# Kernel tuning notes

Hardware: AMD Instinct MI355X
Metric: run time of the kernel (lower is better)

## Reference

```python
import jax, jax.numpy as jnp
import numpy as np

N, D, C, T = 8192, 64, 100, 30  # samples, embedding_dim, n_classes, n_transforms (initialize_radial_flow n_transforms=30)
LOG_EV_CLAMP = 10.0             # EvidenceScaler clamp on log evidence
EV_BUDGET = 0.5 * D * float(np.log(4.0 * np.pi))  # 'normal' evidence budget: 0.5*dim*log(4*pi)


def setup_inputs() -> dict:
    key = jax.random.key(0)
    ks = jax.random.split(key, 8)
    x = jax.random.normal(ks[0], (N, D), dtype=jnp.float32)          # embeddings (base = identity here)
    labels = jax.random.randint(ks[1], (N,), 0, C)                   # int class labels
    freq = jax.random.uniform(ks[2], (C,), dtype=jnp.float32) + 0.1
    freq = freq / freq.sum()                                         # labels_frequency (sums to 1)
    # per-class radial flow params: z0 [C,T,D], alpha' [C,T], beta' [C,T]
    z0 = jax.random.normal(ks[3], (C, T, D), dtype=jnp.float32) * 0.1
    alpha_prime = jax.random.normal(ks[4], (C, T), dtype=jnp.float32) * 0.1
    beta_prime = jax.random.normal(ks[5], (C, T), dtype=jnp.float32) * 0.1
    W = jax.random.normal(ks[6], (D, C), dtype=jnp.float32) / np.sqrt(D)  # CategoricalOutput linear
    b = jnp.zeros((C,), jnp.float32)
    return dict(x=x, labels=labels, labels_frequency=freq, z0=z0,
                alpha_prime=alpha_prime, beta_prime=beta_prime, W=W, b=b)


def _flow_log_prob(x, z0s, aps, bps):
    """Radial normalizing flow log-density (density direction): log N(f(x)) + log|det df/dx|.
    x: [N, D]; z0s: [T, D]; aps, bps: [T]."""
    def step(carry, params):
        z, ld = carry
        z0, ap, bp = params
        alpha = jax.nn.softplus(ap)
        beta = -alpha + jax.nn.softplus(bp)   # beta > -alpha ensures invertibility
        diff = z - z0                          # [N, D]
        r = jnp.linalg.norm(diff, axis=-1)     # [N]
        h = 1.0 / (alpha + r)
        bh = beta * h
        z_new = z + bh[:, None] * diff
        # log|det| = (D-1)*log(1+beta*h) + log(1 + beta*h + beta*h'*r), h' = -h^2
        ld_new = ld + (D - 1) * jnp.log1p(bh) + jnp.log1p(bh * (1.0 - h * r))
        return (z_new, ld_new), None

    init = (x, jnp.zeros(x.shape[0], x.dtype))
    (z, ld), _ = jax.lax.scan(step, init, (z0s, aps, bps))
    base = -0.5 * (D * jnp.log(2.0 * jnp.pi) + jnp.sum(z * z, axis=-1))  # standard normal base
    return base + ld


def reference(x, labels, labels_frequency, z0, alpha_prime, beta_prime, W, b):
    # per-class flow log-probs for ALL samples: [C, N] (dispatch-compute, vectorized over classes)
    lp = jax.vmap(_flow_log_prob, in_axes=(None, 0, 0, 0))(x, z0, alpha_prime, beta_prime)
    # class_specific_log_prob: gather each sample's own-class log-prob (the boolean-mask gather/scatter loop)
    class_lp = jnp.take_along_axis(lp, labels[None, :], axis=0)[0]            # [N]
    # marginalize_log_prob: logsumexp over classes with log class frequencies
    marg = jax.nn.logsumexp(lp + jnp.log(labels_frequency)[:, None], axis=0)  # [N]
    # EvidenceScaler('normal') + clamp, then NatPN Dirichlet posterior update
    log_ev = jnp.minimum(marg + EV_BUDGET, LOG_EV_CLAMP)                      # [N]
    probs = jax.nn.softmax(x @ W + b, axis=-1)                                # expected sufficient statistics
    alpha = 1.0 + jnp.exp(log_ev)[:, None] * probs                            # prior alpha=1 + evidence*stats
    # output: [N, C+1] = [log alpha | class-specific log-prob]
    return jnp.concatenate([jnp.log(alpha), class_lp[:, None]], axis=1)
```

## Files before the change

### kernel.cpp

```cpp
#include <hip/hip_runtime.h>
#include <math.h>

#define N 8192
#define D 64
#define C 100
#define T 30
#define GSTRIDE 32
#define ZROWS 32
#define CROWS 112
#define WSTRIDE 20
#define SB 16

static constexpr float D_LOG_2PI      = 117.62413225019811f;
static constexpr float EV_BUDGET_F    = 80.992775903017304f;
static constexpr float LOG_EV_CLAMP_F = 10.0f;

typedef __attribute__((ext_vector_type(8))) short short8x;
typedef __attribute__((ext_vector_type(4))) float floatx4;

static __device__ __forceinline__ unsigned short f2bf(float f) {
    __bf16 h = (__bf16)f;
    return __builtin_bit_cast(unsigned short, h);
}

__global__ __launch_bounds__(256) void megaprep_kernel(
        const float* __restrict__ x,
        const float* __restrict__ z0,
        const float* __restrict__ ap,
        const float* __restrict__ bp,
        const float* __restrict__ W,
        unsigned short* __restrict__ xbf,
        float* __restrict__ q0,
        float* __restrict__ Gp,
        float* __restrict__ alphas,
        float* __restrict__ betas,
        unsigned short* __restrict__ z0bf,
        unsigned short* __restrict__ wtbf) {
    const int blk = blockIdx.x;

    if (blk < 256) {
        const int r = blk * 32 + (threadIdx.x >> 3);
        const int e = threadIdx.x & 7;
        const float4* xp = (const float4*)(x + (size_t)r * D + e * 8);
        const float4 a = xp[0], b = xp[1];
        short8x o;
        o[0] = f2bf(a.x); o[1] = f2bf(a.y); o[2] = f2bf(a.z); o[3] = f2bf(a.w);
        o[4] = f2bf(b.x); o[5] = f2bf(b.y); o[6] = f2bf(b.z); o[7] = f2bf(b.w);
        *(short8x*)(xbf + (size_t)r * D + e * 8) = o;
        float q = a.x*a.x + a.y*a.y + a.z*a.z + a.w*a.w
                + b.x*b.x + b.y*b.y + b.z*b.z + b.w*b.w;
        q += __shfl_xor(q, 4, 8);
        q += __shfl_xor(q, 2, 8);
        q += __shfl_xor(q, 1, 8);
        if (e == 0) q0[r] = q;
        return;
    }

    if (blk >= 356) {
        const int i = (blk - 356) * 256 + threadIdx.x;
        const int c = i >> 6, d = i & 63;
        wtbf[i] = f2bf(c < C ? W[d * C + c] : 0.0f);
        return;
    }

    const int c = blk - 256;
    __shared__ float z0s[T * D];
    for (int i = threadIdx.x; i < T * D; i += blockDim.x)
        z0s[i] = z0[c * T * D + i];
    __syncthreads();

    for (int idx = threadIdx.x; idx < T * T; idx += blockDim.x) {
        const int u = idx / T, v = idx % T;
        float s = 0.0f;
        #pragma unroll
        for (int d = 0; d < D; ++d)
            s = fmaf(z0s[u * D + d], z0s[v * D + d], s);
        Gp[(size_t)c * T * GSTRIDE + u * GSTRIDE + v] = s;
    }

    for (int i = threadIdx.x; i < ZROWS * D; i += blockDim.x) {
        const int u = i >> 6;
        z0bf[(size_t)c * ZROWS * D + i] = f2bf(u < T ? z0s[u * D + (i & 63)] : 0.0f);
    }

    if (threadIdx.x < T) {
        const float a = ap[c * T + threadIdx.x];
        const float b = bp[c * T + threadIdx.x];
        const float spa = fmaxf(a, 0.0f) + log1pf(expf(-fabsf(a)));
        const float spb = fmaxf(b, 0.0f) + log1pf(expf(-fabsf(b)));
        alphas[c * T + threadIdx.x] = spa;
        betas[c * T + threadIdx.x]  = -spa + spb;
    }
}

__global__ __launch_bounds__(256, 3) void flow_kernel(
        const unsigned short* __restrict__ xbf,
        const float* __restrict__ q0g,
        const unsigned short* __restrict__ z0bf,
        const float* __restrict__ Gp,
        const float* __restrict__ alphas,
        const float* __restrict__ betas,
        float* __restrict__ lp) {
    const int c    = blockIdx.y;
    const int wv   = threadIdx.x >> 6;
    const int ln   = threadIdx.x & 63;
    const int col  = ln & 15;
    const int quad = ln >> 4;
    const int nb   = blockIdx.x * 256 + wv * 64;
    const int n    = nb + ln;

    __shared__ float Gs[T * GSTRIDE];
    __shared__ float ab[64];
    __shared__ float wlds[4][64 * WSTRIDE];

    for (int i = threadIdx.x; i < T * GSTRIDE; i += 256)
        Gs[i] = Gp[(size_t)c * T * GSTRIDE + i];
    if (threadIdx.x < T) ab[threadIdx.x] = alphas[c * T + threadIdx.x];
    else if (threadIdx.x >= 32 && threadIdx.x < 32 + T)
        ab[threadIdx.x] = betas[c * T + (threadIdx.x - 32)];
    __syncthreads();

    const unsigned short* zb = z0bf + (size_t)c * ZROWS * D;
    float w[ZROWS];

    #pragma unroll
    for (int mu = 0; mu < 2; ++mu) {
        const short8x A0 = *(const short8x*)(zb + (mu * 16 + col) * D + quad * 8);
        const short8x A1 = *(const short8x*)(zb + (mu * 16 + col) * D + 32 + quad * 8);
        floatx4 acc[4];
        #pragma unroll
        for (int nt = 0; nt < 4; ++nt) acc[nt] = (floatx4)(0.0f);
        #pragma unroll
        for (int nt = 0; nt < 4; ++nt) {
            const unsigned short* bp_ = xbf + (size_t)(nb + nt * 16 + col) * D + quad * 8;
            const short8x B0 = *(const short8x*)(bp_);
            acc[nt] = __builtin_amdgcn_mfma_f32_16x16x32_bf16(A0, B0, acc[nt], 0, 0, 0);
            const short8x B1 = *(const short8x*)(bp_ + 32);
            acc[nt] = __builtin_amdgcn_mfma_f32_16x16x32_bf16(A1, B1, acc[nt], 0, 0, 0);
        }
        #pragma unroll
        for (int nt = 0; nt < 4; ++nt)
            *(floatx4*)&wlds[wv][(nt * 16 + col) * WSTRIDE + quad * 4] = acc[nt];
        #pragma unroll
        for (int j = 0; j < 4; ++j) {
            const float4 t = *(const float4*)&wlds[wv][ln * WSTRIDE + j * 4];
            w[mu * 16 + 4 * j + 0] = t.x; w[mu * 16 + 4 * j + 1] = t.y;
            w[mu * 16 + 4 * j + 2] = t.z; w[mu * 16 + 4 * j + 3] = t.w;
        }
    }

    float q    = q0g[n];
    float P    = 1.0f;
    float prod = 1.0f;
    float ld   = 0.0f;
    #pragma unroll
    for (int t = 0; t < T; ++t) {
        const float Gtt   = Gs[t * GSTRIDE + t];
        const float alpha = ab[t];
        const float beta  = ab[32 + t];
        const float wt    = P * w[t];
        float r2 = fmaf(-2.0f, wt, q) + Gtt;
        r2 = fmaxf(r2, 0.0f);
        const float r  = __builtin_amdgcn_sqrtf(r2);
        const float h  = __builtin_amdgcn_rcpf(alpha + r);
        const float bh = beta * h;
        const float f  = 1.0f + bh;
        const float f2 = f * f, f4 = f2 * f2, f8 = f4 * f4;
        const float f16 = f8 * f8, f32v = f16 * f16;
        float p = f32v * f16; p *= f8; p *= f4; p *= f2; p *= f;
        p *= fmaf(bh * alpha, h, 1.0f);
        prod *= p;
        if ((t % 6) == 5) { ld += __logf(prod); prod = 1.0f; }
        const float m = bh * f;
        float qn = f2 * q;
        qn = fmaf(m, -2.0f * wt, qn);
        qn = fmaf(bh * bh, Gtt, qn);
        q = qn;
        const float Pn = P * f;
        const float k  = bh * __builtin_amdgcn_rcpf(Pn);
        #pragma unroll
        for (int m4 = 0; m4 < 8; ++m4) {
            if (m4 < (t >> 2)) continue;
            const float4 g = *(const float4*)&Gs[t * GSTRIDE + 4 * m4];
            w[4 * m4 + 0] = fmaf(-k, g.x, w[4 * m4 + 0]);
            w[4 * m4 + 1] = fmaf(-k, g.y, w[4 * m4 + 1]);
            w[4 * m4 + 2] = fmaf(-k, g.z, w[4 * m4 + 2]);
            w[4 * m4 + 3] = fmaf(-k, g.w, w[4 * m4 + 3]);
        }
        P = Pn;
    }
    ld += __logf(prod);

    lp[(size_t)c * N + n] = -0.5f * (D_LOG_2PI + q) + ld;
}

__global__ __launch_bounds__(256) void logits_kernel(
        const unsigned short* __restrict__ xbf,
        const unsigned short* __restrict__ wtbf,
        const float* __restrict__ b,
        float* __restrict__ lgT) {
    const int wv   = threadIdx.x >> 6;
    const int ln   = threadIdx.x & 63;
    const int col  = ln & 15;
    const int quad = ln >> 4;
    const int n0   = (blockIdx.x * 4 + wv) * 16;

    const unsigned short* bp_ = xbf + (size_t)(n0 + col) * D + quad * 8;
    const short8x B0 = *(const short8x*)(bp_);
    const short8x B1 = *(const short8x*)(bp_ + 32);

    #pragma unroll
    for (int ct = 0; ct < 7; ++ct) {
        const unsigned short* apq = wtbf + (size_t)(ct * 16 + col) * D + quad * 8;
        const short8x A0 = *(const short8x*)(apq);
        const short8x A1 = *(const short8x*)(apq + 32);
        floatx4 acc = (floatx4)(0.0f);
        acc = __builtin_amdgcn_mfma_f32_16x16x32_bf16(A0, B0, acc, 0, 0, 0);
        acc = __builtin_amdgcn_mfma_f32_16x16x32_bf16(A1, B1, acc, 0, 0, 0);
        #pragma unroll
        for (int j = 0; j < 4; ++j) {
            const int cc = ct * 16 + quad * 4 + j;
            if (cc < C)
                lgT[(size_t)cc * N + n0 + col] = acc[j] + b[cc];
        }
    }
}

__global__ __launch_bounds__(256) void epilogue_kernel(
        const float* __restrict__ lp,
        const float* __restrict__ lgT,
        const int* __restrict__ labels,
        const float* __restrict__ freq,
        float* __restrict__ out) {
    const int n0  = blockIdx.x * SB;
    const int tid = threadIdx.x;

    __shared__ float lps[SB][101];
    __shared__ float lgs[SB][101];
    __shared__ float lf[C];
    __shared__ int   lbl[SB];

    for (int i = tid; i < C * SB; i += 256) {
        const int cc = i >> 4, s = i & (SB - 1);
        lps[s][cc] = lp[(size_t)cc * N + n0 + s];
        lgs[s][cc] = lgT[(size_t)cc * N + n0 + s];
    }
    if (tid < C) lf[tid] = __logf(freq[tid]);
    if (tid < SB) lbl[tid] = labels[n0 + tid];
    __syncthreads();

    const int s = tid >> 4;
    const int k = tid & 15;
    const int n = n0 + s;

    float lgt[7];
    float lm = -INFINITY;
    float vm = -INFINITY, vs = 0.0f;
    #pragma unroll
    for (int j = 0; j < 7; ++j) {
        const int cc = k + 16 * j;
        if (cc < C) {
            const float v = lps[s][cc] + lf[cc];
            const float m2 = fmaxf(vm, v);
            vs = vs * __expf(vm - m2) + __expf(v - m2);
            vm = m2;
            lgt[j] = lgs[s][cc];
            lm = fmaxf(lm, lgt[j]);
        } else lgt[j] = -INFINITY;
    }

    #pragma unroll
    for (int off = 8; off >= 1; off >>= 1) {
        const float om = __shfl_xor(vm, off, 16);
        const float os = __shfl_xor(vs, off, 16);
        const float m2 = fmaxf(vm, om);
        vs = vs * __expf(vm - m2) + os * __expf(om - m2);
        vm = m2;
        lm = fmaxf(lm, __shfl_xor(lm, off, 16));
    }
    const float marg = vm + __logf(vs);
    const float ev = __expf(fminf(marg + EV_BUDGET_F, LOG_EV_CLAMP_F));

    float ls = 0.0f;
    #pragma unroll
    for (int j = 0; j < 7; ++j)
        if (k + 16 * j < C) ls += __expf(lgt[j] - lm);
    #pragma unroll
    for (int off = 8; off >= 1; off >>= 1)
        ls += __shfl_xor(ls, off, 16);

    const float inv = ev / ls;
    float* __restrict__ outr = out + (size_t)n * (C + 1);
    #pragma unroll
    for (int j = 0; j < 7; ++j) {
        const int cc = k + 16 * j;
        if (cc < C) outr[cc] = log1pf(__expf(lgt[j] - lm) * inv);
    }
    if (k == 0) outr[C] = lps[s][lbl[s]];
}

extern "C" void kernel_launch(void* const* d_in, const int* in_sizes, int n_in,
                              void* d_out, int out_size, void* d_ws, size_t ws_size,
                              hipStream_t stream) {
    const float* x      = (const float*)d_in[0];
    const int*   labels = (const int*)  d_in[1];
    const float* freq   = (const float*)d_in[2];
    const float* z0     = (const float*)d_in[3];
    const float* ap     = (const float*)d_in[4];
    const float* bp     = (const float*)d_in[5];
    const float* W      = (const float*)d_in[6];
    const float* b      = (const float*)d_in[7];
    float* out = (float*)d_out;

    float* ws     = (float*)d_ws;
    float* lp     = ws;
    float* lgT    = lp + (size_t)C * N;
    float* Gp     = lgT + (size_t)C * N;
    float* alphas = Gp + (size_t)C * T * GSTRIDE;
    float* betas  = alphas + (size_t)C * T;
    unsigned short* z0bf = (unsigned short*)(betas + (size_t)C * T);
    unsigned short* xbf  = z0bf + (size_t)C * ZROWS * D;
    unsigned short* wtbf = xbf + (size_t)N * D;
    float* q0     = (float*)(wtbf + (size_t)CROWS * D);

    megaprep_kernel<<<384, 256, 0, stream>>>(x, z0, ap, bp, W,
                                             xbf, q0, Gp, alphas, betas, z0bf, wtbf);
    flow_kernel<<<dim3(N / 256, C), 256, 0, stream>>>(xbf, q0, z0bf, Gp, alphas, betas, lp);
    logits_kernel<<<N / 64, 256, 0, stream>>>(xbf, wtbf, b, lgT);
    epilogue_kernel<<<N / SB, 256, 0, stream>>>(lp, lgT, labels, freq, out);
}
```

Measured before the change: 153.7 us.

## Fuse logits GEMM into epilogue kernel and relax flow kernel occupancy bound

Removes the separate logits kernel. Wave 0 of each epilogue block now computes the 16x112 logits tile with bf16 MFMA directly into shared memory, while the other three waves load the flow log-probs, log frequencies, bias and labels. This drops the C*N logits round trip through global memory and one kernel launch. Separately, the flow kernel's launch bounds go from 3 to 2 blocks per SIMD, which gives the compiler more registers but may lower occupancy.

```diff
diff --git a/kernel.cpp b/kernel.cpp
--- a/kernel.cpp
+++ b/kernel.cpp
@@ -93,7 +93,7 @@
     }
 }
 
-__global__ __launch_bounds__(256, 3) void flow_kernel(
+__global__ __launch_bounds__(256, 2) void flow_kernel(
         const unsigned short* __restrict__ xbf,
         const float* __restrict__ q0g,
         const unsigned short* __restrict__ z0bf,
@@ -194,59 +194,56 @@
     lp[(size_t)c * N + n] = -0.5f * (D_LOG_2PI + q) + ld;
 }
 
-__global__ __launch_bounds__(256) void logits_kernel(
+__global__ __launch_bounds__(256) void epilogue_kernel(
+        const float* __restrict__ lp,
         const unsigned short* __restrict__ xbf,
         const unsigned short* __restrict__ wtbf,
         const float* __restrict__ b,
-        float* __restrict__ lgT) {
-    const int wv   = threadIdx.x >> 6;
-    const int ln   = threadIdx.x & 63;
-    const int col  = ln & 15;
-    const int quad = ln >> 4;
-    const int n0   = (blockIdx.x * 4 + wv) * 16;
-
-    const unsigned short* bp_ = xbf + (size_t)(n0 + col) * D + quad * 8;
-    const short8x B0 = *(const short8x*)(bp_);
-    const short8x B1 = *(const short8x*)(bp_ + 32);
-
-    #pragma unroll
-    for (int ct = 0; ct < 7; ++ct) {
-        const unsigned short* apq = wtbf + (size_t)(ct * 16 + col) * D + quad * 8;
-        const short8x A0 = *(const short8x*)(apq);
-        const short8x A1 = *(const short8x*)(apq + 32);
-        floatx4 acc = (floatx4)(0.0f);
-        acc = __builtin_amdgcn_mfma_f32_16x16x32_bf16(A0, B0, acc, 0, 0, 0);
-        acc = __builtin_amdgcn_mfma_f32_16x16x32_bf16(A1, B1, acc, 0, 0, 0);
-        #pragma unroll
-        for (int j = 0; j < 4; ++j) {
-            const int cc = ct * 16 + quad * 4 + j;
-            if (cc < C)
-                lgT[(size_t)cc * N + n0 + col] = acc[j] + b[cc];
-        }
-    }
-}
-
-__global__ __launch_bounds__(256) void epilogue_kernel(
-        const float* __restrict__ lp,
-        const float* __restrict__ lgT,
         const int* __restrict__ labels,
         const float* __restrict__ freq,
         float* __restrict__ out) {
     const int n0  = blockIdx.x * SB;
     const int tid = threadIdx.x;
+    const int wv  = tid >> 6;
+    const int ln  = tid & 63;
 
     __shared__ float lps[SB][101];
-    __shared__ float lgs[SB][101];
+    __shared__ float lgs[SB][CROWS];
     __shared__ float lf[C];
+    __shared__ float bsm[C];
     __shared__ int   lbl[SB];
 
-    for (int i = tid; i < C * SB; i += 256) {
-        const int cc = i >> 4, s = i & (SB - 1);
-        lps[s][cc] = lp[(size_t)cc * N + n0 + s];
-        lgs[s][cc] = lgT[(size_t)cc * N + n0 + s];
-    }
-    if (tid < C) lf[tid] = __logf(freq[tid]);
-    if (tid < SB) lbl[tid] = labels[n0 + tid];
+    if (wv == 0) {
+        const int col  = ln & 15;
+        const int quad = ln >> 4;
+        const unsigned short* bp_ = xbf + (size_t)(n0 + col) * D + quad * 8;
+        const short8x B0 = *(const short8x*)(bp_);
+        const short8x B1 = *(const short8x*)(bp_ + 32);
+        #pragma unroll
+        for (int ct = 0; ct < 7; ++ct) {
+            const unsigned short* apq = wtbf + (size_t)(ct * 16 + col) * D + quad * 8;
+            const short8x A0 = *(const short8x*)(apq);
+            const short8x A1 = *(const short8x*)(apq + 32);
+            floatx4 acc = (floatx4)(0.0f);
+            acc = __builtin_amdgcn_mfma_f32_16x16x32_bf16(A0, B0, acc, 0, 0, 0);
+            acc = __builtin_amdgcn_mfma_f32_16x16x32_bf16(A1, B1, acc, 0, 0, 0);
+            #pragma unroll
+            for (int j = 0; j < 4; ++j)
+                lgs[col][ct * 16 + quad * 4 + j] = acc[j];
+        }
+    } else {
+        for (int i = tid - 64; i < C * SB; i += 192) {
+            const int cc = i >> 4, s = i & (SB - 1);
+            lps[s][cc] = lp[(size_t)cc * N + n0 + s];
+        }
+        if (tid - 64 < C) {
+            const int t2 = tid - 64;
+            lf[t2]  = __logf(freq[t2]);
+            bsm[t2] = b[t2];
+        }
+        if (tid >= 192 && tid < 192 + SB)
+            lbl[tid - 192] = labels[n0 + (tid - 192)];
+    }
     __syncthreads();
 
     const int s = tid >> 4;
@@ -264,7 +261,7 @@
             const float m2 = fmaxf(vm, v);
             vs = vs * __expf(vm - m2) + __expf(v - m2);
             vm = m2;
-            lgt[j] = lgs[s][cc];
+            lgt[j] = lgs[s][cc] + bsm[cc];
             lm = fmaxf(lm, lgt[j]);
         } else lgt[j] = -INFINITY;
     }
@@ -314,8 +311,7 @@
 
     float* ws     = (float*)d_ws;
     float* lp     = ws;
-    float* lgT    = lp + (size_t)C * N;
-    float* Gp     = lgT + (size_t)C * N;
+    float* Gp     = lp + (size_t)C * N;
     float* alphas = Gp + (size_t)C * T * GSTRIDE;
     float* betas  = alphas + (size_t)C * T;
     unsigned short* z0bf = (unsigned short*)(betas + (size_t)C * T);
@@ -326,6 +322,5 @@
     megaprep_kernel<<<384, 256, 0, stream>>>(x, z0, ap, bp, W,
                                              xbf, q0, Gp, alphas, betas, z0bf, wtbf);
     flow_kernel<<<dim3(N / 256, C), 256, 0, stream>>>(xbf, q0, z0bf, Gp, alphas, betas, lp);
-    logits_kernel<<<N / 64, 256, 0, stream>>>(xbf, wtbf, b, lgT);
-    epilogue_kernel<<<N / SB, 256, 0, stream>>>(lp, lgT, labels, freq, out);
-}
+    epilogue_kernel<<<N / SB, 256, 0, stream>>>(lp, xbf, wtbf, b, labels, freq, out);
+}
```

Result: no change. 151.5 us (-1.4%).
